# Kernel optimization log

Measured on AMD Instinct MI355X. Metric: run time of the kernel, lower is better.

Reference implementation:

```python
import jax, jax.numpy as jnp
import numpy as np

B, S, D = 4, 2048, 1024
H, DK, DV = 16, 64, 64
LN_EPS = 1e-5


def setup_inputs() -> dict:
    key = jax.random.key(0)
    ks = jax.random.split(key, 6)
    x = jax.random.normal(ks[0], (B, S, D), dtype=jnp.float32)
    # causal mask: True = masked position (j > i), broadcast over batch
    causal = jnp.triu(jnp.ones((S, S), dtype=bool), k=1)
    attention_mask = jnp.broadcast_to(causal, (B, S, S))
    scale = 1.0 / np.sqrt(D)
    w_q = jax.random.normal(ks[1], (D, H * DK), dtype=jnp.float32) * scale
    w_k = jax.random.normal(ks[2], (D, H * DK), dtype=jnp.float32) * scale
    w_v = jax.random.normal(ks[3], (D, H * DV), dtype=jnp.float32) * scale
    w_fc = jax.random.normal(ks[4], (H * DV, D), dtype=jnp.float32) * (1.0 / np.sqrt(H * DV))
    ln_gamma = jnp.ones((D,), dtype=jnp.float32)
    ln_beta = jnp.zeros((D,), dtype=jnp.float32)
    return {"x": x, "attention_mask": attention_mask, "w_q": w_q, "w_k": w_k,
            "w_v": w_v, "w_fc": w_fc, "ln_gamma": ln_gamma, "ln_beta": ln_beta}


def _layernorm(y, gamma, beta):
    mu = jnp.mean(y, axis=-1, keepdims=True)
    var = jnp.mean(jnp.square(y - mu), axis=-1, keepdims=True)
    return (y - mu) * jax.lax.rsqrt(var + LN_EPS) * gamma + beta


def reference(x, attention_mask, w_q, w_k, w_v, w_fc, ln_gamma, ln_beta):
    b, s, _ = x.shape
    # projections -> [b, h, s, dk/dv]
    q = (x @ w_q).reshape(b, s, H, DK).transpose(0, 2, 1, 3)
    k = (x @ w_k).reshape(b, s, H, DK).transpose(0, 2, 1, 3)
    v = (x @ w_v).reshape(b, s, H, DV).transpose(0, 2, 1, 3)
    # scaled dot-product attention with mask (True -> -1e9)
    scores = jnp.einsum('bhqd,bhkd->bhqk', q, k) / np.sqrt(DK)
    scores = jnp.where(attention_mask[:, None, :, :], jnp.float32(-1e9), scores)
    attn = jax.nn.softmax(scores, axis=-1)
    context = jnp.einsum('bhqk,bhkd->bhqd', attn, v)
    context = context.transpose(0, 2, 1, 3).reshape(b, s, H * DV)
    output = context @ w_fc
    out = _layernorm(output + x, ln_gamma, ln_beta)
    return out, attn
```

## Files before the change

kernel.cpp:

```cpp
#include <hip/hip_runtime.h>
#include <stdint.h>

#define S_LEN 2048
#define NHEAD 16

typedef short short8 __attribute__((ext_vector_type(8)));
typedef float f32x4 __attribute__((ext_vector_type(4)));
typedef unsigned short u16;

typedef __attribute__((address_space(1))) uint32_t AS1u32;
typedef __attribute__((address_space(3))) uint32_t AS3u32;

#define MFMA16(a, b, c) __builtin_amdgcn_mfma_f32_16x16x32_bf16((a), (b), (c), 0, 0, 0)

__device__ __forceinline__ void gload16(const void* g, void* l) {
  __builtin_amdgcn_global_load_lds((AS1u32*)g, (AS3u32*)l, 16, 0, 0);
}

__device__ __forceinline__ u16 f2bf(float f) {
  union { float f; uint32_t u; } c; c.f = f;
  return (u16)((c.u + 0x7fffu + ((c.u >> 16) & 1u)) >> 16);
}
__device__ __forceinline__ float bf2f(u16 h) {
  union { uint32_t u; float f; } c; c.u = ((uint32_t)h) << 16;
  return c.f;
}

__global__ __launch_bounds__(256) void prep_kernel(
    const float* __restrict__ x, u16* __restrict__ xb,
    const float* __restrict__ w0, const float* __restrict__ w1,
    const float* __restrict__ w2, const float* __restrict__ w3,
    u16* __restrict__ qkvT, u16* __restrict__ fcT) {
  __shared__ float t[32][33];
  int bid = blockIdx.x;
  if (bid < 8192) {
    size_t i = ((size_t)bid * 256 + threadIdx.x) * 4;
    f32x4 v = *(const f32x4*)(x + i);
    union { u16 h[4]; uint2 d; } o;
    o.h[0] = f2bf(v[0]); o.h[1] = f2bf(v[1]); o.h[2] = f2bf(v[2]); o.h[3] = f2bf(v[3]);
    *(uint2*)(xb + i) = o.d;
    return;
  }
  int r = bid - 8192;
  int z = r >> 10; r &= 1023;
  int bx = r & 31, by = r >> 5;
  const float* w = (z == 0) ? w0 : (z == 1) ? w1 : (z == 2) ? w2 : w3;
  u16* o = (z == 3) ? fcT : qkvT + (size_t)z * 1048576;
  float scale = (z == 0) ? 0.125f : 1.0f;
  int n0 = bx * 32, k0 = by * 32;
  int tx = threadIdx.x & 31, ty = threadIdx.x >> 5;
#pragma unroll
  for (int i = 0; i < 4; ++i) {
    int k = ty * 4 + i;
    t[k][tx] = w[(size_t)(k0 + k) * 1024 + n0 + tx];
  }
  __syncthreads();
#pragma unroll
  for (int i = 0; i < 4; ++i) {
    int n = ty * 4 + i;
    o[(size_t)(n0 + n) * 1024 + k0 + tx] = f2bf(t[tx][n] * scale);
  }
}

__device__ __forceinline__ void gemm_stage(const char* Ab, const char* Bb, u16* As, u16* Bs,
                                           int m0, int n0, int kbyte, int tid) {
#pragma unroll
  for (int i = 0; i < 2; ++i) {
    int cid = i * 256 + tid;
    int row = cid >> 2, c = cid & 3;
    int off = kbyte + ((c ^ ((row >> 1) & 3)) << 4);
    gload16(Ab + (size_t)(m0 + row) * 2048 + off, (char*)As + i * 4096 + (tid & ~63) * 16);
    gload16(Bb + (size_t)(n0 + row) * 2048 + off, (char*)Bs + i * 4096 + (tid & ~63) * 16);
  }
}

__global__ __launch_bounds__(256) void gemm_bt_kernel(
    const u16* __restrict__ A, const u16* __restrict__ BT,
    void* __restrict__ out, int mode) {
  __shared__ u16 sh[128 * 128];
  u16* As = sh;
  u16* Bs = sh + 4096;
  const int tid = threadIdx.x;
  const int lane = tid & 63, wv = tid >> 6;
  const int l15 = lane & 15, h16 = lane >> 4;
  const int wr = wv >> 1, wc = wv & 1;
  const int m0 = blockIdx.x * 128, n0 = blockIdx.y * 128;
  const char* Ab = (const char*)A;
  const char* Bb = (const char*)BT;

  f32x4 acc[4][4];
#pragma unroll
  for (int i = 0; i < 4; ++i)
#pragma unroll
    for (int j = 0; j < 4; ++j) acc[i][j] = (f32x4){0.f, 0.f, 0.f, 0.f};

  gemm_stage(Ab, Bb, As, Bs, m0, n0, 0, tid);
  for (int kt = 0; kt < 32; ++kt) {
    __syncthreads();
    short8 a[4], b[4];
#pragma unroll
    for (int mf = 0; mf < 4; ++mf) {
      int row = wr * 64 + mf * 16 + l15;
      a[mf] = *(const short8*)((const char*)As + row * 64 + ((h16 ^ ((row >> 1) & 3)) << 4));
    }
#pragma unroll
    for (int nf = 0; nf < 4; ++nf) {
      int row = wc * 64 + nf * 16 + l15;
      b[nf] = *(const short8*)((const char*)Bs + row * 64 + ((h16 ^ ((row >> 1) & 3)) << 4));
    }
#pragma unroll
    for (int mf = 0; mf < 4; ++mf)
#pragma unroll
      for (int nf = 0; nf < 4; ++nf)
        acc[mf][nf] = MFMA16(a[mf], b[nf], acc[mf][nf]);
    __syncthreads();
    if (kt + 1 < 32) gemm_stage(Ab, Bb, As, Bs, m0, n0, (kt + 1) * 64, tid);
  }

  if (mode == 0) {
    u16* o = (u16*)out;
#pragma unroll
    for (int mf = 0; mf < 4; ++mf)
#pragma unroll
      for (int nf = 0; nf < 4; ++nf)
#pragma unroll
        for (int r = 0; r < 4; ++r) {
          int row = wr * 64 + mf * 16 + 4 * h16 + r;
          int col = wc * 64 + nf * 16 + l15;
          *(u16*)((char*)sh + row * 256 + (((col >> 3) ^ (row & 7)) << 4) + (col & 7) * 2) =
              f2bf(acc[mf][nf][r]);
        }
    __syncthreads();
    int row = tid >> 1, hf = tid & 1;
    int m = m0 + row;
    int bb = m >> 11, s = m & 2047;
    int n_base = n0 + hf * 64;
    int z = n_base >> 10, nn = n_base & 1023, hh = nn >> 6;
    u16* dst = o + (size_t)z * 8388608 + (((size_t)(bb * NHEAD + hh) * S_LEN + s) << 6);
#pragma unroll
    for (int i = 0; i < 8; ++i) {
      int ch = hf * 8 + i;
      short8 v = *(const short8*)((const char*)sh + row * 256 + ((ch ^ (row & 7)) << 4));
      *(short8*)(dst + i * 8) = v;
    }
  } else {
    float* o = (float*)out;
#pragma unroll
    for (int mf = 0; mf < 4; ++mf)
#pragma unroll
      for (int nf = 0; nf < 4; ++nf)
#pragma unroll
        for (int r = 0; r < 4; ++r) {
          int m = m0 + wr * 64 + mf * 16 + 4 * h16 + r;
          int n = n0 + wc * 64 + nf * 16 + l15;
          o[(size_t)m * 1024 + n] = acc[mf][nf][r];
        }
  }
}

__global__ __launch_bounds__(256) void transpose_v_kernel(
    const u16* __restrict__ v, u16* __restrict__ vT) {
  __shared__ u16 t[64][80];
  int bh = blockIdx.y, s0 = blockIdx.x * 64;
  int tid = threadIdx.x;
  int sl = tid >> 2, c = tid & 3;
  const u16* src = v + (size_t)bh * S_LEN * 64 + (size_t)(s0 + sl) * 64 + c * 16;
  short8 a = *(const short8*)src;
  short8 b = *(const short8*)(src + 8);
#pragma unroll
  for (int j = 0; j < 8; ++j) {
    t[c * 16 + j][sl] = (u16)a[j];
    t[c * 16 + 8 + j][sl] = (u16)b[j];
  }
  __syncthreads();
  int dv = tid >> 2, c2 = tid & 3;
  u16* dst = vT + (size_t)bh * 64 * S_LEN + (size_t)dv * S_LEN + s0 + c2 * 16;
  *(short8*)dst = *(const short8*)&t[dv][c2 * 16];
  *(short8*)(dst + 8) = *(const short8*)&t[dv][c2 * 16 + 8];
}

__device__ __forceinline__ void stage_qk(const char* base, int row0, u16* dst, int tid) {
#pragma unroll
  for (int i = 0; i < 2; ++i) {
    int cid = i * 512 + tid;
    int row = cid >> 3, c = cid & 7;
    gload16(base + (size_t)(row0 + row) * 128 + ((c ^ (row & 7)) << 4),
            (char*)dst + i * 8192 + (tid & ~63) * 16);
  }
}
__device__ __forceinline__ void stage_v(const char* Vb, int kv0, u16* dst, int tid) {
#pragma unroll
  for (int i = 0; i < 2; ++i) {
    int cid = i * 512 + tid;
    int row = cid >> 4, c = cid & 15;
    gload16(Vb + (size_t)row * 4096 + (size_t)kv0 * 2 + ((c ^ (row & 7)) << 4),
            (char*)dst + i * 8192 + (tid & ~63) * 16);
  }
}

__global__ __launch_bounds__(512) void denom_kernel(
    const u16* __restrict__ Q, const u16* __restrict__ K, float* __restrict__ rinv) {
  __shared__ u16 Qs[128 * 64];
  __shared__ u16 Ks[2][128 * 64];
  const int tid = threadIdx.x;
  const int lane = tid & 63, wv = tid >> 6;
  const int l15 = lane & 15, h16 = lane >> 4;
  const int w16 = wv * 16;
  const int qt = 15 - blockIdx.x, bh = blockIdx.y;
  const int q0 = qt * 128;
  const char* Qb = (const char*)(Q + (size_t)bh * S_LEN * 64);
  const char* Kb = (const char*)(K + (size_t)bh * S_LEN * 64);

  stage_qk(Qb, q0, Qs, tid);
  stage_qk(Kb, 0, Ks[0], tid);
  __syncthreads();
  short8 qf[2];
  {
    int row = w16 + l15;
    qf[0] = *(const short8*)((const char*)Qs + row * 128 + ((h16 ^ (row & 7)) << 4));
    qf[1] = *(const short8*)((const char*)Qs + row * 128 + (((4 + h16) ^ (row & 7)) << 4));
  }
  __syncthreads();

  float lsum[4] = {0.f, 0.f, 0.f, 0.f};
  int cur = 0;
  for (int t = 0; t <= qt; ++t) {
    if (t + 1 <= qt) stage_qk(Kb, (t + 1) * 128, Ks[cur ^ 1], tid);
    const char* Kc = (const char*)Ks[cur];
    f32x4 sc[8];
#pragma unroll
    for (int nf = 0; nf < 8; ++nf) sc[nf] = (f32x4){0.f, 0.f, 0.f, 0.f};
#pragma unroll
    for (int ks = 0; ks < 2; ++ks)
#pragma unroll
      for (int nf = 0; nf < 8; ++nf) {
        int row = nf * 16 + l15;
        short8 kb = *(const short8*)(Kc + row * 128 + (((ks * 4 + h16) ^ (row & 7)) << 4));
        sc[nf] = MFMA16(qf[ks], kb, sc[nf]);
      }
    if (t == qt) {
#pragma unroll
      for (int nf = 0; nf < 8; ++nf)
#pragma unroll
        for (int r = 0; r < 4; ++r)
          if (nf * 16 + l15 > w16 + 4 * h16 + r) sc[nf][r] = -1e30f;
    }
#pragma unroll
    for (int nf = 0; nf < 8; ++nf)
#pragma unroll
      for (int r = 0; r < 4; ++r) lsum[r] += __expf(sc[nf][r]);
    __syncthreads();
    cur ^= 1;
  }
#pragma unroll
  for (int r = 0; r < 4; ++r) {
    float v = lsum[r];
    v += __shfl_xor(v, 1);
    v += __shfl_xor(v, 2);
    v += __shfl_xor(v, 4);
    v += __shfl_xor(v, 8);
    lsum[r] = v;
  }
  if (l15 == 0) {
    f32x4 o = {1.f / lsum[0], 1.f / lsum[1], 1.f / lsum[2], 1.f / lsum[3]};
    *(f32x4*)(rinv + (size_t)bh * S_LEN + q0 + w16 + 4 * h16) = o;
  }
}

__global__ __launch_bounds__(512) void emit_kernel(
    const u16* __restrict__ Q, const u16* __restrict__ K, const u16* __restrict__ VT,
    const float* __restrict__ rinv, float* __restrict__ attn, u16* __restrict__ ctx) {
  __shared__ u16 Ks[2][128 * 64];
  __shared__ u16 Vs[64 * 128];
  __shared__ u16 Ps[128 * 128];

  const int tid = threadIdx.x;
  const int lane = tid & 63, wv = tid >> 6;
  const int l15 = lane & 15, h16 = lane >> 4;
  const int w16 = wv * 16;
  const int qt = 15 - blockIdx.x, bh = blockIdx.y;
  const int q0 = qt * 128;

  const char* Qb = (const char*)(Q + (size_t)bh * S_LEN * 64);
  const char* Kb = (const char*)(K + (size_t)bh * S_LEN * 64);
  const char* Vb = (const char*)(VT + (size_t)bh * 64 * S_LEN);
  float* attb = attn + (size_t)bh * S_LEN * S_LEN;

  stage_qk(Qb, q0, Ps, tid);
  stage_qk(Kb, 0, Ks[0], tid);
  __syncthreads();
  short8 qf[2];
  {
    int row = w16 + l15;
    qf[0] = *(const short8*)((const char*)Ps + row * 128 + ((h16 ^ (row & 7)) << 4));
    qf[1] = *(const short8*)((const char*)Ps + row * 128 + (((4 + h16) ^ (row & 7)) << 4));
  }
  f32x4 ri = *(const f32x4*)(rinv + (size_t)bh * S_LEN + q0 + w16 + 4 * h16);
  __syncthreads();

  f32x4 cacc[4];
#pragma unroll
  for (int nf = 0; nf < 4; ++nf) cacc[nf] = (f32x4){0.f, 0.f, 0.f, 0.f};

  int cur = 0;
  for (int t = 0; t <= qt; ++t) {
    const int kv0 = t * 128;
    stage_v(Vb, kv0, Vs, tid);
    const char* Kc = (const char*)Ks[cur];
    f32x4 sc[8];
#pragma unroll
    for (int nf = 0; nf < 8; ++nf) sc[nf] = (f32x4){0.f, 0.f, 0.f, 0.f};
#pragma unroll
    for (int ks = 0; ks < 2; ++ks)
#pragma unroll
      for (int nf = 0; nf < 8; ++nf) {
        int row = nf * 16 + l15;
        short8 kb = *(const short8*)(Kc + row * 128 + (((ks * 4 + h16) ^ (row & 7)) << 4));
        sc[nf] = MFMA16(qf[ks], kb, sc[nf]);
      }
    if (t == qt) {
#pragma unroll
      for (int nf = 0; nf < 8; ++nf)
#pragma unroll
        for (int r = 0; r < 4; ++r)
          if (nf * 16 + l15 > w16 + 4 * h16 + r) sc[nf][r] = -1e30f;
    }
#pragma unroll
    for (int nf = 0; nf < 8; ++nf)
#pragma unroll
      for (int r = 0; r < 4; ++r) {
        float p = __expf(sc[nf][r]) * ri[r];
        int rowL = w16 + 4 * h16 + r;
        int chunk = 2 * nf + (l15 >> 3);
        *(u16*)((char*)Ps + rowL * 256 + ((chunk ^ (rowL & 7)) << 4) + (l15 & 7) * 2) = f2bf(p);
      }
    __syncthreads();
    if (t + 1 <= qt) stage_qk(Kb, kv0 + 128, Ks[cur ^ 1], tid);
#pragma unroll
    for (int ks = 0; ks < 4; ++ks) {
      int rowP = w16 + l15;
      short8 pa = *(const short8*)((const char*)Ps + rowP * 256 + (((ks * 4 + h16) ^ (rowP & 7)) << 4));
#pragma unroll
      for (int nf = 0; nf < 4; ++nf) {
        int rowV = nf * 16 + l15;
        short8 vbf = *(const short8*)((const char*)Vs + rowV * 256 + (((ks * 4 + h16) ^ (rowV & 7)) << 4));
        cacc[nf] = MFMA16(pa, vbf, cacc[nf]);
      }
    }
    {
      int row = tid >> 2, sub = tid & 3;
      const char* prow = (const char*)Ps + row * 256;
      float* arow = attb + (size_t)(q0 + row) * S_LEN + kv0;
#pragma unroll
      for (int c8 = 0; c8 < 4; ++c8) {
        int chunk = sub + 4 * c8;
        short8 pv = *(const short8*)(prow + ((chunk ^ (row & 7)) << 4));
        f32x4 f0 = {bf2f((u16)pv[0]), bf2f((u16)pv[1]), bf2f((u16)pv[2]), bf2f((u16)pv[3])};
        f32x4 f1 = {bf2f((u16)pv[4]), bf2f((u16)pv[5]), bf2f((u16)pv[6]), bf2f((u16)pv[7])};
        *(f32x4*)(arow + chunk * 8) = f0;
        *(f32x4*)(arow + chunk * 8 + 4) = f1;
      }
    }
    __syncthreads();
    cur ^= 1;
  }

  for (int kvt = qt + 1; kvt < 16; ++kvt) {
    const int kv0 = kvt * 128;
    int row = tid >> 2, sub = tid & 3;
    float* arow = attb + (size_t)(q0 + row) * S_LEN + kv0;
    f32x4 z = {0.f, 0.f, 0.f, 0.f};
#pragma unroll
    for (int c8 = 0; c8 < 4; ++c8) {
      int chunk = sub + 4 * c8;
      *(f32x4*)(arow + chunk * 8) = z;
      *(f32x4*)(arow + chunk * 8 + 4) = z;
    }
  }

  {
    int b = bh >> 4, hh = bh & 15;
#pragma unroll
    for (int nf = 0; nf < 4; ++nf)
#pragma unroll
      for (int r = 0; r < 4; ++r) {
        int qrow = q0 + w16 + 4 * h16 + r;
        ctx[((size_t)b * S_LEN + qrow) * 1024 + hh * 64 + nf * 16 + l15] = f2bf(cacc[nf][r]);
      }
  }
}

__global__ __launch_bounds__(256) void ln_kernel(float* __restrict__ io,
                                                 const float* __restrict__ x,
                                                 const float* __restrict__ gamma,
                                                 const float* __restrict__ beta) {
  int row = blockIdx.x, tid = threadIdx.x;
  size_t base = (size_t)row * 1024 + tid * 4;
  f32x4 p = *(const f32x4*)(io + base);
  f32x4 xv = *(const f32x4*)(x + base);
  f32x4 y;
  float s1 = 0.f, s2 = 0.f;
#pragma unroll
  for (int j = 0; j < 4; ++j) {
    y[j] = p[j] + xv[j];
    s1 += y[j];
    s2 += y[j] * y[j];
  }
#pragma unroll
  for (int off = 1; off <= 32; off <<= 1) {
    s1 += __shfl_xor(s1, off);
    s2 += __shfl_xor(s2, off);
  }
  __shared__ float r1[4], r2[4];
  int w = tid >> 6;
  if ((tid & 63) == 0) { r1[w] = s1; r2[w] = s2; }
  __syncthreads();
  float S1 = r1[0] + r1[1] + r1[2] + r1[3];
  float S2 = r2[0] + r2[1] + r2[2] + r2[3];
  float mu = S1 * (1.f / 1024.f);
  float var = S2 * (1.f / 1024.f) - mu * mu;
  float rs = rsqrtf(var + 1e-5f);
  f32x4 g = *(const f32x4*)(gamma + tid * 4);
  f32x4 bt = *(const f32x4*)(beta + tid * 4);
  f32x4 o;
#pragma unroll
  for (int j = 0; j < 4; ++j) o[j] = (y[j] - mu) * rs * g[j] + bt[j];
  *(f32x4*)(io + base) = o;
}

extern "C" void kernel_launch(void* const* d_in, const int* in_sizes, int n_in,
                              void* d_out, int out_size, void* d_ws, size_t ws_size,
                              hipStream_t stream) {
  (void)in_sizes; (void)n_in; (void)out_size; (void)ws_size;
  const float* x = (const float*)d_in[0];
  const float* wq = (const float*)d_in[2];
  const float* wk = (const float*)d_in[3];
  const float* wv = (const float*)d_in[4];
  const float* wfc = (const float*)d_in[5];
  const float* gamma = (const float*)d_in[6];
  const float* beta = (const float*)d_in[7];

  char* ws = (char*)d_ws;
  u16* xb = (u16*)ws;
  u16* wqkvT = (u16*)(ws + (16u << 20));
  u16* wfcT = (u16*)(ws + (22u << 20));
  u16* qkvb = (u16*)(ws + (24u << 20));
  u16* qb = qkvb;
  u16* kb = qkvb + (size_t)8388608;
  u16* vb = qkvb + (size_t)16777216;
  u16* vT = (u16*)(ws + (72u << 20));
  float* rinvp = (float*)(ws + (56u << 20));
  u16* ctx = xb;

  float* outp = (float*)d_out;
  float* attnp = outp + (size_t)4 * 2048 * 1024;

  prep_kernel<<<12288, 256, 0, stream>>>(x, xb, wq, wk, wv, wfc, wqkvT, wfcT);
  gemm_bt_kernel<<<dim3(64, 24), 256, 0, stream>>>(xb, wqkvT, qkvb, 0);
  transpose_v_kernel<<<dim3(32, 64), 256, 0, stream>>>(vb, vT);
  denom_kernel<<<dim3(16, 64), 512, 0, stream>>>(qb, kb, rinvp);
  emit_kernel<<<dim3(16, 64), 512, 0, stream>>>(qb, kb, vT, rinvp, attnp, ctx);
  gemm_bt_kernel<<<dim3(64, 8), 256, 0, stream>>>(ctx, wfcT, outp, 1);
  ln_kernel<<<8192, 256, 0, stream>>>(outp, x, gamma, beta);
}
```

Measured before the change: 487.3 us.

## Fuse V transpose into QKV GEMM and merge denom/emit attention passes

The QKV GEMM epilogue now writes the V output already transposed through LDS, which removes the separate transpose kernel and one round trip of V through memory. The denominator and emit kernels are merged into one attention kernel. Each block handles a pair of causal query tiles (qt and 15-qt) to balance work, and runs the denominator pass in reverse so the diagonal K tile is left in LDS for the emit pass. This cuts kernel launches and the rinv buffer, at the cost of half as many blocks and longer-running blocks.

```diff
diff --git a/kernel.cpp b/kernel.cpp
--- a/kernel.cpp
+++ b/kernel.cpp
@@ -76,7 +76,7 @@
 
 __global__ __launch_bounds__(256) void gemm_bt_kernel(
     const u16* __restrict__ A, const u16* __restrict__ BT,
-    void* __restrict__ out, int mode) {
+    void* __restrict__ out, void* __restrict__ outv, int mode) {
   __shared__ u16 sh[128 * 128];
   u16* As = sh;
   u16* Bs = sh + 4096;
@@ -117,7 +117,7 @@
     if (kt + 1 < 32) gemm_stage(Ab, Bb, As, Bs, m0, n0, (kt + 1) * 64, tid);
   }
 
-  if (mode == 0) {
+  if (mode == 0 && n0 < 2048) {
     u16* o = (u16*)out;
 #pragma unroll
     for (int mf = 0; mf < 4; ++mf)
@@ -143,6 +143,31 @@
       short8 v = *(const short8*)((const char*)sh + row * 256 + ((ch ^ (row & 7)) << 4));
       *(short8*)(dst + i * 8) = v;
     }
+  } else if (mode == 0) {
+    u16* o = (u16*)outv;
+#pragma unroll
+    for (int mf = 0; mf < 4; ++mf)
+#pragma unroll
+      for (int nf = 0; nf < 4; ++nf)
+#pragma unroll
+        for (int r = 0; r < 4; ++r) {
+          int row = wr * 64 + mf * 16 + 4 * h16 + r;
+          int col = wc * 64 + nf * 16 + l15;
+          *(u16*)((char*)sh + col * 256 + (((row >> 3) ^ (col & 7)) << 4) + (row & 7) * 2) =
+              f2bf(acc[mf][nf][r]);
+        }
+    __syncthreads();
+    int col = tid >> 1, half = tid & 1;
+    int bb = m0 >> 11, s0 = (m0 & 2047) + half * 64;
+    int nn = n0 - 2048 + col;
+    int hh = nn >> 6, dv = nn & 63;
+    u16* dst = o + ((size_t)(bb * NHEAD + hh) * 64 + dv) * S_LEN + s0;
+    const char* base = (const char*)sh + col * 256;
+#pragma unroll
+    for (int i = 0; i < 8; ++i) {
+      int ch = (half * 8 + i) ^ (col & 7);
+      *(short8*)(dst + i * 8) = *(const short8*)(base + (ch << 4));
+    }
   } else {
     float* o = (float*)out;
 #pragma unroll
@@ -158,27 +183,6 @@
   }
 }
 
-__global__ __launch_bounds__(256) void transpose_v_kernel(
-    const u16* __restrict__ v, u16* __restrict__ vT) {
-  __shared__ u16 t[64][80];
-  int bh = blockIdx.y, s0 = blockIdx.x * 64;
-  int tid = threadIdx.x;
-  int sl = tid >> 2, c = tid & 3;
-  const u16* src = v + (size_t)bh * S_LEN * 64 + (size_t)(s0 + sl) * 64 + c * 16;
-  short8 a = *(const short8*)src;
-  short8 b = *(const short8*)(src + 8);
-#pragma unroll
-  for (int j = 0; j < 8; ++j) {
-    t[c * 16 + j][sl] = (u16)a[j];
-    t[c * 16 + 8 + j][sl] = (u16)b[j];
-  }
-  __syncthreads();
-  int dv = tid >> 2, c2 = tid & 3;
-  u16* dst = vT + (size_t)bh * 64 * S_LEN + (size_t)dv * S_LEN + s0 + c2 * 16;
-  *(short8*)dst = *(const short8*)&t[dv][c2 * 16];
-  *(short8*)(dst + 8) = *(const short8*)&t[dv][c2 * 16 + 8];
-}
-
 __device__ __forceinline__ void stage_qk(const char* base, int row0, u16* dst, int tid) {
 #pragma unroll
   for (int i = 0; i < 2; ++i) {
@@ -198,46 +202,50 @@
   }
 }
 
-__global__ __launch_bounds__(512) void denom_kernel(
-    const u16* __restrict__ Q, const u16* __restrict__ K, float* __restrict__ rinv) {
-  __shared__ u16 Qs[128 * 64];
-  __shared__ u16 Ks[2][128 * 64];
-  const int tid = threadIdx.x;
+__device__ __forceinline__ void qk_tile(const char* Kc, const short8* qf,
+                                        f32x4* sc, int l15, int h16) {
+#pragma unroll
+  for (int nf = 0; nf < 8; ++nf) sc[nf] = (f32x4){0.f, 0.f, 0.f, 0.f};
+#pragma unroll
+  for (int ks = 0; ks < 2; ++ks)
+#pragma unroll
+    for (int nf = 0; nf < 8; ++nf) {
+      int row = nf * 16 + l15;
+      short8 kb = *(const short8*)(Kc + row * 128 + (((ks * 4 + h16) ^ (row & 7)) << 4));
+      sc[nf] = MFMA16(qf[ks], kb, sc[nf]);
+    }
+}
+
+__device__ __forceinline__ void attn_one(
+    const u16* __restrict__ Q, const u16* __restrict__ K, const u16* __restrict__ VT,
+    float* __restrict__ attn, u16* __restrict__ ctx, int qt, int bh, int tid,
+    u16 (*Ks)[128 * 64], u16* Vs, u16* Ps) {
   const int lane = tid & 63, wv = tid >> 6;
   const int l15 = lane & 15, h16 = lane >> 4;
   const int w16 = wv * 16;
-  const int qt = 15 - blockIdx.x, bh = blockIdx.y;
   const int q0 = qt * 128;
   const char* Qb = (const char*)(Q + (size_t)bh * S_LEN * 64);
   const char* Kb = (const char*)(K + (size_t)bh * S_LEN * 64);
-
-  stage_qk(Qb, q0, Qs, tid);
-  stage_qk(Kb, 0, Ks[0], tid);
+  const char* Vb = (const char*)(VT + (size_t)bh * 64 * S_LEN);
+  float* attb = attn + (size_t)bh * S_LEN * S_LEN;
+
+  stage_qk(Qb, q0, Ps, tid);
+  stage_qk(Kb, q0, Ks[0], tid);
   __syncthreads();
   short8 qf[2];
   {
     int row = w16 + l15;
-    qf[0] = *(const short8*)((const char*)Qs + row * 128 + ((h16 ^ (row & 7)) << 4));
-    qf[1] = *(const short8*)((const char*)Qs + row * 128 + (((4 + h16) ^ (row & 7)) << 4));
+    qf[0] = *(const short8*)((const char*)Ps + row * 128 + ((h16 ^ (row & 7)) << 4));
+    qf[1] = *(const short8*)((const char*)Ps + row * 128 + (((4 + h16) ^ (row & 7)) << 4));
   }
   __syncthreads();
 
   float lsum[4] = {0.f, 0.f, 0.f, 0.f};
   int cur = 0;
-  for (int t = 0; t <= qt; ++t) {
-    if (t + 1 <= qt) stage_qk(Kb, (t + 1) * 128, Ks[cur ^ 1], tid);
-    const char* Kc = (const char*)Ks[cur];
+  for (int t = qt; t >= 0; --t) {
+    if (t > 0) stage_qk(Kb, (t - 1) * 128, Ks[cur ^ 1], tid);
     f32x4 sc[8];
-#pragma unroll
-    for (int nf = 0; nf < 8; ++nf) sc[nf] = (f32x4){0.f, 0.f, 0.f, 0.f};
-#pragma unroll
-    for (int ks = 0; ks < 2; ++ks)
-#pragma unroll
-      for (int nf = 0; nf < 8; ++nf) {
-        int row = nf * 16 + l15;
-        short8 kb = *(const short8*)(Kc + row * 128 + (((ks * 4 + h16) ^ (row & 7)) << 4));
-        sc[nf] = MFMA16(qf[ks], kb, sc[nf]);
-      }
+    qk_tile((const char*)Ks[cur], qf, sc, l15, h16);
     if (t == qt) {
 #pragma unroll
       for (int nf = 0; nf < 8; ++nf)
@@ -252,6 +260,8 @@
     __syncthreads();
     cur ^= 1;
   }
+  cur ^= 1;
+  f32x4 ri;
 #pragma unroll
   for (int r = 0; r < 4; ++r) {
     float v = lsum[r];
@@ -259,65 +269,18 @@
     v += __shfl_xor(v, 2);
     v += __shfl_xor(v, 4);
     v += __shfl_xor(v, 8);
-    lsum[r] = v;
-  }
-  if (l15 == 0) {
-    f32x4 o = {1.f / lsum[0], 1.f / lsum[1], 1.f / lsum[2], 1.f / lsum[3]};
-    *(f32x4*)(rinv + (size_t)bh * S_LEN + q0 + w16 + 4 * h16) = o;
-  }
-}
-
-__global__ __launch_bounds__(512) void emit_kernel(
-    const u16* __restrict__ Q, const u16* __restrict__ K, const u16* __restrict__ VT,
-    const float* __restrict__ rinv, float* __restrict__ attn, u16* __restrict__ ctx) {
-  __shared__ u16 Ks[2][128 * 64];
-  __shared__ u16 Vs[64 * 128];
-  __shared__ u16 Ps[128 * 128];
-
-  const int tid = threadIdx.x;
-  const int lane = tid & 63, wv = tid >> 6;
-  const int l15 = lane & 15, h16 = lane >> 4;
-  const int w16 = wv * 16;
-  const int qt = 15 - blockIdx.x, bh = blockIdx.y;
-  const int q0 = qt * 128;
-
-  const char* Qb = (const char*)(Q + (size_t)bh * S_LEN * 64);
-  const char* Kb = (const char*)(K + (size_t)bh * S_LEN * 64);
-  const char* Vb = (const char*)(VT + (size_t)bh * 64 * S_LEN);
-  float* attb = attn + (size_t)bh * S_LEN * S_LEN;
-
-  stage_qk(Qb, q0, Ps, tid);
-  stage_qk(Kb, 0, Ks[0], tid);
-  __syncthreads();
-  short8 qf[2];
-  {
-    int row = w16 + l15;
-    qf[0] = *(const short8*)((const char*)Ps + row * 128 + ((h16 ^ (row & 7)) << 4));
-    qf[1] = *(const short8*)((const char*)Ps + row * 128 + (((4 + h16) ^ (row & 7)) << 4));
-  }
-  f32x4 ri = *(const f32x4*)(rinv + (size_t)bh * S_LEN + q0 + w16 + 4 * h16);
-  __syncthreads();
+    ri[r] = 1.0f / v;
+  }
 
   f32x4 cacc[4];
 #pragma unroll
   for (int nf = 0; nf < 4; ++nf) cacc[nf] = (f32x4){0.f, 0.f, 0.f, 0.f};
 
-  int cur = 0;
   for (int t = 0; t <= qt; ++t) {
     const int kv0 = t * 128;
     stage_v(Vb, kv0, Vs, tid);
-    const char* Kc = (const char*)Ks[cur];
     f32x4 sc[8];
-#pragma unroll
-    for (int nf = 0; nf < 8; ++nf) sc[nf] = (f32x4){0.f, 0.f, 0.f, 0.f};
-#pragma unroll
-    for (int ks = 0; ks < 2; ++ks)
-#pragma unroll
-      for (int nf = 0; nf < 8; ++nf) {
-        int row = nf * 16 + l15;
-        short8 kb = *(const short8*)(Kc + row * 128 + (((ks * 4 + h16) ^ (row & 7)) << 4));
-        sc[nf] = MFMA16(qf[ks], kb, sc[nf]);
-      }
+    qk_tile((const char*)Ks[cur], qf, sc, l15, h16);
     if (t == qt) {
 #pragma unroll
       for (int nf = 0; nf < 8; ++nf)
@@ -335,7 +298,7 @@
         *(u16*)((char*)Ps + rowL * 256 + ((chunk ^ (rowL & 7)) << 4) + (l15 & 7) * 2) = f2bf(p);
       }
     __syncthreads();
-    if (t + 1 <= qt) stage_qk(Kb, kv0 + 128, Ks[cur ^ 1], tid);
+    if (t < qt) stage_qk(Kb, kv0 + 128, Ks[cur ^ 1], tid);
 #pragma unroll
     for (int ks = 0; ks < 4; ++ks) {
       int rowP = w16 + l15;
@@ -388,6 +351,18 @@
         ctx[((size_t)b * S_LEN + qrow) * 1024 + hh * 64 + nf * 16 + l15] = f2bf(cacc[nf][r]);
       }
   }
+}
+
+__global__ __launch_bounds__(512) void attn2_kernel(
+    const u16* __restrict__ Q, const u16* __restrict__ K, const u16* __restrict__ VT,
+    float* __restrict__ attn, u16* __restrict__ ctx) {
+  __shared__ u16 Ks[2][128 * 64];
+  __shared__ u16 Vs[64 * 128];
+  __shared__ u16 Ps[128 * 128];
+  const int tid = threadIdx.x;
+  const int bh = blockIdx.y;
+  attn_one(Q, K, VT, attn, ctx, 15 - blockIdx.x, bh, tid, Ks, Vs, Ps);
+  attn_one(Q, K, VT, attn, ctx, blockIdx.x, bh, tid, Ks, Vs, Ps);
 }
 
 __global__ __launch_bounds__(256) void ln_kernel(float* __restrict__ io,
@@ -444,22 +419,18 @@
   u16* xb = (u16*)ws;
   u16* wqkvT = (u16*)(ws + (16u << 20));
   u16* wfcT = (u16*)(ws + (22u << 20));
-  u16* qkvb = (u16*)(ws + (24u << 20));
-  u16* qb = qkvb;
-  u16* kb = qkvb + (size_t)8388608;
-  u16* vb = qkvb + (size_t)16777216;
-  u16* vT = (u16*)(ws + (72u << 20));
-  float* rinvp = (float*)(ws + (56u << 20));
+  u16* qkb = (u16*)(ws + (24u << 20));
+  u16* qb = qkb;
+  u16* kb = qkb + (size_t)8388608;
+  u16* vT = (u16*)(ws + (56u << 20));
   u16* ctx = xb;
 
   float* outp = (float*)d_out;
   float* attnp = outp + (size_t)4 * 2048 * 1024;
 
   prep_kernel<<<12288, 256, 0, stream>>>(x, xb, wq, wk, wv, wfc, wqkvT, wfcT);
-  gemm_bt_kernel<<<dim3(64, 24), 256, 0, stream>>>(xb, wqkvT, qkvb, 0);
-  transpose_v_kernel<<<dim3(32, 64), 256, 0, stream>>>(vb, vT);
-  denom_kernel<<<dim3(16, 64), 512, 0, stream>>>(qb, kb, rinvp);
-  emit_kernel<<<dim3(16, 64), 512, 0, stream>>>(qb, kb, vT, rinvp, attnp, ctx);
-  gemm_bt_kernel<<<dim3(64, 8), 256, 0, stream>>>(ctx, wfcT, outp, 1);
+  gemm_bt_kernel<<<dim3(64, 24), 256, 0, stream>>>(xb, wqkvT, qkb, vT, 0);
+  attn2_kernel<<<dim3(8, 64), 512, 0, stream>>>(qb, kb, vT, attnp, ctx);
+  gemm_bt_kernel<<<dim3(64, 8), 256, 0, stream>>>(ctx, wfcT, outp, nullptr, 1);
   ln_kernel<<<8192, 256, 0, stream>>>(outp, x, gamma, beta);
 }
```

Measured after the change: 477.1 us. 1.02x faster.
